# Performance work log

Measured on AMD Instinct MI355X. Metric: run time of the kernel, lower is better.

The kernel has to match this reference:

```python
import jax, jax.numpy as jnp
import numpy as np

TAU = 3.0      # time horizon (init arg tau)
FIX = 0.2      # correction gain (init arg fix)


def setup_inputs() -> dict:
    key = jax.random.key(0)
    k1, k2, k3, k4, k5 = jax.random.split(key, 5)
    B, N, K = 256, 1024, 32
    p_cur = jax.random.normal(k1, (B, N, 2), dtype=jnp.float32) * 10.0   # positions (meters)
    v_cur = jax.random.normal(k2, (B, N, 2), dtype=jnp.float32)          # previous velocities
    v_desire = jax.random.normal(k3, (B, N, 2), dtype=jnp.float32)       # desired velocities
    near_ped_idx = jax.random.randint(k4, (B, N, K), 0, N, dtype=jnp.int32)
    neigh_ped_mask = jax.random.randint(k5, (B, N, K), 0, 2).astype(jnp.float32)
    return {
        "p_cur": p_cur,
        "v_cur": v_cur,
        "v_desire": v_desire,
        "near_ped_idx": near_ped_idx,
        "neigh_ped_mask": neigh_ped_mask,
        "collision_threshold": 1,
    }


def reference(p_cur, v_cur, v_desire, near_ped_idx, neigh_ped_mask, collision_threshold):
    # Gather neighbor positions/velocities: (B,N,K,2). vmap over batch avoids
    # materializing the (B,N,N,2) expanded tensor the torch code logically builds.
    gather = jax.vmap(lambda arr, idx: arr[idx])
    neighbors_pos = gather(p_cur, near_ped_idx)
    neighbors_vel = gather(v_cur, near_ped_idx)

    mask = neigh_ped_mask[..., None]                      # (B,N,K,1)
    neighbors_pos = neighbors_pos * mask
    neighbors_vel = neighbors_vel * mask

    rel_pos = p_cur[:, :, None, :] - neighbors_pos        # (B,N,K,2)
    rel_vel = v_desire[:, :, None, :] - neighbors_vel     # (B,N,K,2)

    dot_pos_vel = jnp.sum(rel_pos * rel_vel, axis=-1)     # (B,N,K)
    dot_vel_vel = jnp.sum(rel_vel * rel_vel, axis=-1) + 1e-6
    t_min = dot_pos_vel / (dot_vel_vel + 1e-6)
    t_min = jnp.where(jnp.isnan(t_min), TAU, t_min)
    t_clamp = jnp.clip(t_min, 0.0, TAU)

    min_dist = jnp.linalg.norm(rel_pos + t_clamp[..., None] * rel_vel, axis=-1)
    min_dist = jnp.where(jnp.isnan(min_dist), 1e6, min_dist)

    collision_mask = (min_dist < collision_threshold) & (neigh_ped_mask != 0)

    # 90-degree rotated rel_pos as collision normal
    normal = jnp.stack([-rel_pos[..., 1], rel_pos[..., 0]], axis=-1)   # (B,N,K,2)
    denom = jnp.linalg.norm(normal, axis=-1, keepdims=True)
    normal = jnp.where(collision_mask[..., None], normal / (denom + 1e-6), 0.0)

    correction = jnp.sum(normal, axis=2)                  # (B,N,2)
    correction = jnp.nan_to_num(correction, nan=0.0)
    v_next = v_desire + correction * FIX
    return v_next
```

## Files before the change

### kernel.cpp

```cpp
#include <hip/hip_runtime.h>

#define TAU 3.0f
#define FIX 0.2f
#define NPED 1024
#define PEDS_PER_BLOCK 128
#define BLOCK 512
#define PASSES (PEDS_PER_BLOCK / (BLOCK / 8))

__global__ __launch_bounds__(BLOCK, 8) void rvo_kernel(
    const float* __restrict__ p_cur,
    const float* __restrict__ v_cur,
    const float* __restrict__ v_desire,
    const int*   __restrict__ near_idx,
    const float* __restrict__ mask_arr,
    const int*   __restrict__ cth,
    float*       __restrict__ out,
    int N)
{
    __shared__ float4 table[NPED];

    const int tid    = threadIdx.x;
    const int bpb    = N / PEDS_PER_BLOCK;
    const int batch  = blockIdx.x / bpb;
    const int pbase  = (blockIdx.x % bpb) * PEDS_PER_BLOCK;

    const float2* pb2 = (const float2*)(p_cur) + (size_t)batch * N;
    const float2* vb2 = (const float2*)(v_cur) + (size_t)batch * N;
    #pragma unroll
    for (int n = tid; n < NPED; n += BLOCK) {
        float2 pp = pb2[n];
        float2 vv = vb2[n];
        table[n] = make_float4(pp.x, pp.y, vv.x, vv.y);
    }
    __syncthreads();

    const float thr2 = (float)cth[0] * (float)cth[0];

    const int sub  = tid & 7;
    const int pgrp = tid >> 3;

    #pragma unroll
    for (int pass = 0; pass < PASSES; ++pass) {
        const int ped  = pbase + pass * (BLOCK / 8) + pgrp;
        const size_t pair = (size_t)batch * N + ped;

        const float4 self = table[ped];
        const float2 vd   = ((const float2*)v_desire)[pair];
        const float px = self.x, py = self.y;
        const float vdx = vd.x, vdy = vd.y;

        const int4   i4 = ((const int4*)near_idx)[pair * 8 + sub];
        const float4 m4 = ((const float4*)mask_arr)[pair * 8 + sub];
        const int   idxs[4] = {i4.x, i4.y, i4.z, i4.w};
        const float ms[4]   = {m4.x, m4.y, m4.z, m4.w};

        float nx = 0.0f, ny = 0.0f;
        #pragma unroll
        for (int j = 0; j < 4; ++j) {
            const float4 nb = table[idxs[j]];
            const float m = ms[j];
            const float rpx = px  - nb.x * m;
            const float rpy = py  - nb.y * m;
            const float rvx = vdx - nb.z * m;
            const float rvy = vdy - nb.w * m;

            const float dpv = rpx * rvx + rpy * rvy;
            const float dvv = rvx * rvx + rvy * rvy + 2e-6f;
            float t = dpv * __builtin_amdgcn_rcpf(dvv);
            t = fminf(fmaxf(t, 0.0f), TAU);

            const float cx = rpx + t * rvx;
            const float cy = rpy + t * rvy;
            const float md2 = cx * cx + cy * cy;

            const float s = rpx * rpx + rpy * rpy;
            const bool coll = (md2 < thr2) && (m != 0.0f) && (s > 0.0f);
            const float inv = __builtin_amdgcn_rsqf(s);
            const float sel = coll ? inv : 0.0f;
            nx = fmaf(-rpy, sel, nx);
            ny = fmaf( rpx, sel, ny);
        }

        #pragma unroll
        for (int d = 4; d > 0; d >>= 1) {
            nx += __shfl_down(nx, d, 8);
            ny += __shfl_down(ny, d, 8);
        }

        if (sub == 0) {
            ((float2*)out)[pair] = make_float2(fmaf(nx, FIX, vdx),
                                               fmaf(ny, FIX, vdy));
        }
    }
}

extern "C" void kernel_launch(void* const* d_in, const int* in_sizes, int n_in,
                              void* d_out, int out_size, void* d_ws, size_t ws_size,
                              hipStream_t stream) {
    const float* p_cur    = (const float*)d_in[0];
    const float* v_cur    = (const float*)d_in[1];
    const float* v_desire = (const float*)d_in[2];
    const int*   near_idx = (const int*)d_in[3];
    const float* mask_arr = (const float*)d_in[4];
    const int*   cth      = (const int*)d_in[5];
    float*       out      = (float*)d_out;

    const int N  = NPED;
    const int BN = in_sizes[0] / 2;
    dim3 block(BLOCK);
    dim3 grid(BN / PEDS_PER_BLOCK);
    rvo_kernel<<<grid, block, 0, stream>>>(p_cur, v_cur, v_desire, near_idx,
                                           mask_arr, cth, out, N);
}
```

Measured before the change: 110.6 us.

## Double the peds per block, prefetch next pass's indices and masks

Each block now handles 256 pedestrians instead of 128, so the shared position/velocity table is loaded once per 256 peds and there are half as many blocks. The neighbour-index and mask vectors for the next pass are loaded before the current pass computes, overlapping global loads with math. The arithmetic is rewritten with explicit FMAs, and the mask is applied as a multiply rather than a boolean test. The occupancy hint in launch_bounds is dropped, which may raise register use. The mask-multiply only matches the original when masks are 0 or 1.

```diff
diff --git a/kernel.cpp b/kernel.cpp
--- a/kernel.cpp
+++ b/kernel.cpp
@@ -3,11 +3,12 @@
 #define TAU 3.0f
 #define FIX 0.2f
 #define NPED 1024
-#define PEDS_PER_BLOCK 128
+#define PEDS_PER_BLOCK 256
 #define BLOCK 512
-#define PASSES (PEDS_PER_BLOCK / (BLOCK / 8))
+#define GROUPS (BLOCK / 8)
+#define PASSES (PEDS_PER_BLOCK / GROUPS)
 
-__global__ __launch_bounds__(BLOCK, 8) void rvo_kernel(
+__global__ __launch_bounds__(BLOCK) void rvo_kernel(
     const float* __restrict__ p_cur,
     const float* __restrict__ v_cur,
     const float* __restrict__ v_desire,
@@ -38,45 +39,59 @@
 
     const int sub  = tid & 7;
     const int pgrp = tid >> 3;
+    const size_t base = (size_t)batch * N + pbase + pgrp;
+
+    const int4*   idx4  = (const int4*)near_idx;
+    const float4* msk4  = (const float4*)mask_arr;
+    const float2* vd2   = (const float2*)v_desire;
+
+    int4   i4 = idx4[base * 8 + sub];
+    float4 m4 = msk4[base * 8 + sub];
 
     #pragma unroll
     for (int pass = 0; pass < PASSES; ++pass) {
-        const int ped  = pbase + pass * (BLOCK / 8) + pgrp;
-        const size_t pair = (size_t)batch * N + ped;
+        const int4   ci = i4;
+        const float4 cm = m4;
+        if (pass + 1 < PASSES) {
+            const size_t npair = base + (size_t)(pass + 1) * GROUPS;
+            i4 = idx4[npair * 8 + sub];
+            m4 = msk4[npair * 8 + sub];
+        }
+
+        const int ped  = pbase + pass * GROUPS + pgrp;
+        const size_t pair = base + (size_t)pass * GROUPS;
 
         const float4 self = table[ped];
-        const float2 vd   = ((const float2*)v_desire)[pair];
+        const float2 vd   = vd2[pair];
         const float px = self.x, py = self.y;
         const float vdx = vd.x, vdy = vd.y;
 
-        const int4   i4 = ((const int4*)near_idx)[pair * 8 + sub];
-        const float4 m4 = ((const float4*)mask_arr)[pair * 8 + sub];
-        const int   idxs[4] = {i4.x, i4.y, i4.z, i4.w};
-        const float ms[4]   = {m4.x, m4.y, m4.z, m4.w};
+        const int   idxs[4] = {ci.x, ci.y, ci.z, ci.w};
+        const float ms[4]   = {cm.x, cm.y, cm.z, cm.w};
 
         float nx = 0.0f, ny = 0.0f;
         #pragma unroll
         for (int j = 0; j < 4; ++j) {
             const float4 nb = table[idxs[j]];
             const float m = ms[j];
-            const float rpx = px  - nb.x * m;
-            const float rpy = py  - nb.y * m;
-            const float rvx = vdx - nb.z * m;
-            const float rvy = vdy - nb.w * m;
+            const float rpx = fmaf(-m, nb.x, px);
+            const float rpy = fmaf(-m, nb.y, py);
+            const float rvx = fmaf(-m, nb.z, vdx);
+            const float rvy = fmaf(-m, nb.w, vdy);
 
-            const float dpv = rpx * rvx + rpy * rvy;
-            const float dvv = rvx * rvx + rvy * rvy + 2e-6f;
+            const float dpv = fmaf(rpx, rvx, rpy * rvy);
+            const float dvv = fmaf(rvx, rvx, fmaf(rvy, rvy, 2e-6f));
             float t = dpv * __builtin_amdgcn_rcpf(dvv);
             t = fminf(fmaxf(t, 0.0f), TAU);
 
-            const float cx = rpx + t * rvx;
-            const float cy = rpy + t * rvy;
-            const float md2 = cx * cx + cy * cy;
+            const float cx = fmaf(t, rvx, rpx);
+            const float cy = fmaf(t, rvy, rpy);
+            const float md2 = fmaf(cx, cx, cy * cy);
 
-            const float s = rpx * rpx + rpy * rpy;
-            const bool coll = (md2 < thr2) && (m != 0.0f) && (s > 0.0f);
-            const float inv = __builtin_amdgcn_rsqf(s);
-            const float sel = coll ? inv : 0.0f;
+            const float s = fmaf(rpx, rpx, rpy * rpy);
+            const float sel0 = (s > 0.0f) ? __builtin_amdgcn_rsqf(s) : 0.0f;
+            const float w    = (md2 < thr2) ? m : 0.0f;
+            const float sel  = sel0 * w;
             nx = fmaf(-rpy, sel, nx);
             ny = fmaf( rpx, sel, ny);
         }
```

Measured after the change: 112.0 us. No clear change (+1.3%).
